# Performance work log

Measured on AMD Instinct MI355X. Metric: run time of the kernel, lower is better.

The kernel has to match this reference:

```python
import jax, jax.numpy as jnp
import numpy as np

DX = 0.1  # grid spacing (init arg dx); dy == dx
NX = 4096
NY = 4096


def _pad_bc(X, left, right, top, bottom):
    # X: [1, 1, Nx, Ny]; pad last axis with left/right values, then second-to-last with top/bottom.
    B, C, Nx, Ny = X.shape
    l = jnp.broadcast_to(left, (B, C, Nx, 1)).astype(X.dtype)
    r = jnp.broadcast_to(right, (B, C, Nx, 1)).astype(X.dtype)
    X = jnp.concatenate([l, X, r], axis=3)
    t = jnp.broadcast_to(top, (B, C, 1, Ny + 2)).astype(X.dtype)
    bo = jnp.broadcast_to(bottom, (B, C, 1, Ny + 2)).astype(X.dtype)
    return jnp.concatenate([t, X, bo], axis=2)


def _laplacian(Xp):
    # 5-point stencil, equivalent to conv2d with [[0,1,0],[1,-4,1],[0,1,0]]/dx^2 (valid padding).
    inv_dx2 = 1.0 / (DX * DX)
    return (
        Xp[:, :, :-2, 1:-1]
        + Xp[:, :, 2:, 1:-1]
        + Xp[:, :, 1:-1, :-2]
        + Xp[:, :, 1:-1, 2:]
        - 4.0 * Xp[:, :, 1:-1, 1:-1]
    ) * inv_dx2


def setup_inputs() -> dict:
    key = jax.random.key(0)
    k1, k2 = jax.random.split(key)
    state = jax.random.normal(k1, (1, 2, NX, NY), dtype=jnp.float32)
    bc = jax.random.uniform(k2, (1, 2, 4), dtype=jnp.float32)
    a_org = jnp.asarray(-2.0, dtype=jnp.float32)
    b_org = jnp.asarray(-2.0, dtype=jnp.float32)
    k_org = jnp.asarray(-2.0, dtype=jnp.float32)
    return {"state": state, "bc": bc, "a_org": a_org, "b_org": b_org, "k_org": k_org}


def reference(state, bc, a_org, b_org, k_org):
    a = jax.nn.sigmoid(a_org) * 0.01
    b = jax.nn.sigmoid(b_org) * 0.01
    k = jax.nn.sigmoid(k_org) * 0.01

    U = state[:, :1]  # [1,1,Nx,Ny]
    V = state[:, 1:]

    U_ = _pad_bc(U, bc[0, 0, 0], bc[0, 0, 1], bc[0, 0, 2], bc[0, 0, 3])
    V_ = _pad_bc(V, bc[0, 1, 0], bc[0, 1, 1], bc[0, 1, 2], bc[0, 1, 3])

    delta_u = _laplacian(U_)
    delta_v = _laplacian(V_)

    dUdt = a * delta_u + U - U ** 3 - V - k
    dVdt = b * delta_v + U - V
    return jnp.concatenate([dUdt, dVdt], axis=1)
```

## Files before the change

kernel.cpp:

```cpp
#include <hip/hip_runtime.h>

#define NXD 4096
#define NYD 4096

typedef float f32x4 __attribute__((ext_vector_type(4)));

__global__ __launch_bounds__(256) void DiffReactParamPDE_85478439125433_kernel(
    const float* __restrict__ state,
    const float* __restrict__ bc,
    const float* __restrict__ a_org,
    const float* __restrict__ b_org,
    const float* __restrict__ k_org,
    float* __restrict__ out)
{
    const float inv_dx2 = 100.0f;

    const int lane = threadIdx.x & 63;
    const int j0 = (blockIdx.x * 256 + threadIdx.x) * 4;
    const int i0 = blockIdx.y * 2;

    const float* __restrict__ U = state;
    const float* __restrict__ V = state + (size_t)NXD * NYD;
    float* __restrict__ dU = out;
    float* __restrict__ dV = out + (size_t)NXD * NYD;

    const int rT = (i0 == 0) ? 0 : i0 - 1;
    const int rB = (i0 + 2 >= NXD) ? NXD - 1 : i0 + 2;

#define LD4(P, ROW) (*(const float4*)((P) + (size_t)(ROW) * NYD + j0))
    float4 um = LD4(U, rT);
    float4 u0 = LD4(U, i0);
    float4 u1 = LD4(U, i0 + 1);
    float4 up = LD4(U, rB);
    float4 vm = LD4(V, rT);
    float4 v0 = LD4(V, i0);
    float4 v1 = LD4(V, i0 + 1);
    float4 vp = LD4(V, rB);
#undef LD4

    const float uL = bc[0], uR = bc[1], uT = bc[2], uB = bc[3];
    const float vL = bc[4], vR = bc[5], vT = bc[6], vB = bc[7];

    float eLu0 = uL, eLu1 = uL, eLv0 = vL, eLv1 = vL;
    float eRu0 = uR, eRu1 = uR, eRv0 = vR, eRv1 = vR;
    if (lane == 0 && j0 > 0) {
        eLu0 = U[(size_t)i0 * NYD + j0 - 1];
        eLu1 = U[(size_t)(i0 + 1) * NYD + j0 - 1];
        eLv0 = V[(size_t)i0 * NYD + j0 - 1];
        eLv1 = V[(size_t)(i0 + 1) * NYD + j0 - 1];
    }
    if (lane == 63 && j0 + 4 < NYD) {
        eRu0 = U[(size_t)i0 * NYD + j0 + 4];
        eRu1 = U[(size_t)(i0 + 1) * NYD + j0 + 4];
        eRv0 = V[(size_t)i0 * NYD + j0 + 4];
        eRv1 = V[(size_t)(i0 + 1) * NYD + j0 + 4];
    }

    const float a = 0.01f / (1.0f + expf(-a_org[0]));
    const float b = 0.01f / (1.0f + expf(-b_org[0]));
    const float k = 0.01f / (1.0f + expf(-k_org[0]));

    if (i0 == 0) {
        um = make_float4(uT, uT, uT, uT);
        vm = make_float4(vT, vT, vT, vT);
    }
    if (i0 + 2 >= NXD) {
        up = make_float4(uB, uB, uB, uB);
        vp = make_float4(vB, vB, vB, vB);
    }

    {
        float ulft = __shfl_up(u0.w, 1);   if (lane == 0)  ulft = eLu0;
        float urgt = __shfl_down(u0.x, 1); if (lane == 63) urgt = eRu0;
        float vlft = __shfl_up(v0.w, 1);   if (lane == 0)  vlft = eLv0;
        float vrgt = __shfl_down(v0.x, 1); if (lane == 63) vrgt = eRv0;

        const float lu0 = (um.x + u1.x + ulft + u0.y - 4.0f * u0.x) * inv_dx2;
        const float lu1 = (um.y + u1.y + u0.x + u0.z - 4.0f * u0.y) * inv_dx2;
        const float lu2 = (um.z + u1.z + u0.y + u0.w - 4.0f * u0.z) * inv_dx2;
        const float lu3 = (um.w + u1.w + u0.z + urgt - 4.0f * u0.w) * inv_dx2;

        const float lv0 = (vm.x + v1.x + vlft + v0.y - 4.0f * v0.x) * inv_dx2;
        const float lv1 = (vm.y + v1.y + v0.x + v0.z - 4.0f * v0.y) * inv_dx2;
        const float lv2 = (vm.z + v1.z + v0.y + v0.w - 4.0f * v0.z) * inv_dx2;
        const float lv3 = (vm.w + v1.w + v0.z + vrgt - 4.0f * v0.w) * inv_dx2;

        f32x4 duo, dvo;
        duo.x = a * lu0 + u0.x - u0.x * u0.x * u0.x - v0.x - k;
        duo.y = a * lu1 + u0.y - u0.y * u0.y * u0.y - v0.y - k;
        duo.z = a * lu2 + u0.z - u0.z * u0.z * u0.z - v0.z - k;
        duo.w = a * lu3 + u0.w - u0.w * u0.w * u0.w - v0.w - k;

        dvo.x = b * lv0 + u0.x - v0.x;
        dvo.y = b * lv1 + u0.y - v0.y;
        dvo.z = b * lv2 + u0.z - v0.z;
        dvo.w = b * lv3 + u0.w - v0.w;

        const size_t bo = (size_t)i0 * NYD + j0;
        __builtin_nontemporal_store(duo, (f32x4*)(dU + bo));
        __builtin_nontemporal_store(dvo, (f32x4*)(dV + bo));
    }

    {
        float ulft = __shfl_up(u1.w, 1);   if (lane == 0)  ulft = eLu1;
        float urgt = __shfl_down(u1.x, 1); if (lane == 63) urgt = eRu1;
        float vlft = __shfl_up(v1.w, 1);   if (lane == 0)  vlft = eLv1;
        float vrgt = __shfl_down(v1.x, 1); if (lane == 63) vrgt = eRv1;

        const float lu0 = (u0.x + up.x + ulft + u1.y - 4.0f * u1.x) * inv_dx2;
        const float lu1 = (u0.y + up.y + u1.x + u1.z - 4.0f * u1.y) * inv_dx2;
        const float lu2 = (u0.z + up.z + u1.y + u1.w - 4.0f * u1.z) * inv_dx2;
        const float lu3 = (u0.w + up.w + u1.z + urgt - 4.0f * u1.w) * inv_dx2;

        const float lv0 = (v0.x + vp.x + vlft + v1.y - 4.0f * v1.x) * inv_dx2;
        const float lv1 = (v0.y + vp.y + v1.x + v1.z - 4.0f * v1.y) * inv_dx2;
        const float lv2 = (v0.z + vp.z + v1.y + v1.w - 4.0f * v1.z) * inv_dx2;
        const float lv3 = (v0.w + vp.w + v1.z + vrgt - 4.0f * v1.w) * inv_dx2;

        f32x4 duo, dvo;
        duo.x = a * lu0 + u1.x - u1.x * u1.x * u1.x - v1.x - k;
        duo.y = a * lu1 + u1.y - u1.y * u1.y * u1.y - v1.y - k;
        duo.z = a * lu2 + u1.z - u1.z * u1.z * u1.z - v1.z - k;
        duo.w = a * lu3 + u1.w - u1.w * u1.w * u1.w - v1.w - k;

        dvo.x = b * lv0 + u1.x - v1.x;
        dvo.y = b * lv1 + u1.y - v1.y;
        dvo.z = b * lv2 + u1.z - v1.z;
        dvo.w = b * lv3 + u1.w - v1.w;

        const size_t bo = (size_t)(i0 + 1) * NYD + j0;
        __builtin_nontemporal_store(duo, (f32x4*)(dU + bo));
        __builtin_nontemporal_store(dvo, (f32x4*)(dV + bo));
    }
}

extern "C" void kernel_launch(void* const* d_in, const int* in_sizes, int n_in,
                              void* d_out, int out_size, void* d_ws, size_t ws_size,
                              hipStream_t stream) {
    const float* state = (const float*)d_in[0];
    const float* bc    = (const float*)d_in[1];
    const float* a_org = (const float*)d_in[2];
    const float* b_org = (const float*)d_in[3];
    const float* k_org = (const float*)d_in[4];
    float* out = (float*)d_out;

    dim3 block(256, 1, 1);
    dim3 grid(NYD / (4 * 256), NXD / 2, 1);
    DiffReactParamPDE_85478439125433_kernel<<<grid, block, 0, stream>>>(
        state, bc, a_org, b_org, k_org, out);
}
```

Measured before the change: 236.5 us.

## Cover full rows per block and exchange horizontal halos via shared memory

Each block of 1024 threads now spans an entire 4096-wide row pair, so left/right neighbours come from shared memory instead of wavefront shuffles plus scattered scalar global loads at wave edges. This removes the extra uncoalesced edge loads and the per-wave boundary special-casing. In exchange it adds a 32 KB shared buffer, a block-wide barrier, and larger blocks that may lower occupancy on a bandwidth-bound kernel.

```diff
diff --git a/kernel.cpp b/kernel.cpp
--- a/kernel.cpp
+++ b/kernel.cpp
@@ -5,7 +5,7 @@
 
 typedef float f32x4 __attribute__((ext_vector_type(4)));
 
-__global__ __launch_bounds__(256) void DiffReactParamPDE_85478439125433_kernel(
+__global__ __launch_bounds__(1024) void DiffReactParamPDE_85478439125433_kernel(
     const float* __restrict__ state,
     const float* __restrict__ bc,
     const float* __restrict__ a_org,
@@ -15,9 +15,9 @@
 {
     const float inv_dx2 = 100.0f;
 
-    const int lane = threadIdx.x & 63;
-    const int j0 = (blockIdx.x * 256 + threadIdx.x) * 4;
-    const int i0 = blockIdx.y * 2;
+    const int tid = threadIdx.x;
+    const int j0  = tid * 4;
+    const int i0  = blockIdx.x * 2;
 
     const float* __restrict__ U = state;
     const float* __restrict__ V = state + (size_t)NXD * NYD;
@@ -41,24 +41,27 @@
     const float uL = bc[0], uR = bc[1], uT = bc[2], uB = bc[3];
     const float vL = bc[4], vR = bc[5], vT = bc[6], vB = bc[7];
 
-    float eLu0 = uL, eLu1 = uL, eLv0 = vL, eLv1 = vL;
-    float eRu0 = uR, eRu1 = uR, eRv0 = vR, eRv1 = vR;
-    if (lane == 0 && j0 > 0) {
-        eLu0 = U[(size_t)i0 * NYD + j0 - 1];
-        eLu1 = U[(size_t)(i0 + 1) * NYD + j0 - 1];
-        eLv0 = V[(size_t)i0 * NYD + j0 - 1];
-        eLv1 = V[(size_t)(i0 + 1) * NYD + j0 - 1];
-    }
-    if (lane == 63 && j0 + 4 < NYD) {
-        eRu0 = U[(size_t)i0 * NYD + j0 + 4];
-        eRu1 = U[(size_t)(i0 + 1) * NYD + j0 + 4];
-        eRv0 = V[(size_t)i0 * NYD + j0 + 4];
-        eRv1 = V[(size_t)(i0 + 1) * NYD + j0 + 4];
-    }
-
     const float a = 0.01f / (1.0f + expf(-a_org[0]));
     const float b = 0.01f / (1.0f + expf(-b_org[0]));
     const float k = 0.01f / (1.0f + expf(-k_org[0]));
+
+    __shared__ float sx[8][1024];
+    sx[0][tid] = u0.x;  sx[1][tid] = u0.w;
+    sx[2][tid] = u1.x;  sx[3][tid] = u1.w;
+    sx[4][tid] = v0.x;  sx[5][tid] = v0.w;
+    sx[6][tid] = v1.x;  sx[7][tid] = v1.w;
+    __syncthreads();
+
+    const int tm = (tid == 0)    ? 0    : tid - 1;
+    const int tp = (tid == 1023) ? 1023 : tid + 1;
+    float ulft0 = (tid == 0)    ? uL : sx[1][tm];
+    float urgt0 = (tid == 1023) ? uR : sx[0][tp];
+    float ulft1 = (tid == 0)    ? uL : sx[3][tm];
+    float urgt1 = (tid == 1023) ? uR : sx[2][tp];
+    float vlft0 = (tid == 0)    ? vL : sx[5][tm];
+    float vrgt0 = (tid == 1023) ? vR : sx[4][tp];
+    float vlft1 = (tid == 0)    ? vL : sx[7][tm];
+    float vrgt1 = (tid == 1023) ? vR : sx[6][tp];
 
     if (i0 == 0) {
         um = make_float4(uT, uT, uT, uT);
@@ -70,20 +73,15 @@
     }
 
     {
-        float ulft = __shfl_up(u0.w, 1);   if (lane == 0)  ulft = eLu0;
-        float urgt = __shfl_down(u0.x, 1); if (lane == 63) urgt = eRu0;
-        float vlft = __shfl_up(v0.w, 1);   if (lane == 0)  vlft = eLv0;
-        float vrgt = __shfl_down(v0.x, 1); if (lane == 63) vrgt = eRv0;
+        const float lu0 = (um.x + u1.x + ulft0 + u0.y - 4.0f * u0.x) * inv_dx2;
+        const float lu1 = (um.y + u1.y + u0.x  + u0.z - 4.0f * u0.y) * inv_dx2;
+        const float lu2 = (um.z + u1.z + u0.y  + u0.w - 4.0f * u0.z) * inv_dx2;
+        const float lu3 = (um.w + u1.w + u0.z  + urgt0 - 4.0f * u0.w) * inv_dx2;
 
-        const float lu0 = (um.x + u1.x + ulft + u0.y - 4.0f * u0.x) * inv_dx2;
-        const float lu1 = (um.y + u1.y + u0.x + u0.z - 4.0f * u0.y) * inv_dx2;
-        const float lu2 = (um.z + u1.z + u0.y + u0.w - 4.0f * u0.z) * inv_dx2;
-        const float lu3 = (um.w + u1.w + u0.z + urgt - 4.0f * u0.w) * inv_dx2;
-
-        const float lv0 = (vm.x + v1.x + vlft + v0.y - 4.0f * v0.x) * inv_dx2;
-        const float lv1 = (vm.y + v1.y + v0.x + v0.z - 4.0f * v0.y) * inv_dx2;
-        const float lv2 = (vm.z + v1.z + v0.y + v0.w - 4.0f * v0.z) * inv_dx2;
-        const float lv3 = (vm.w + v1.w + v0.z + vrgt - 4.0f * v0.w) * inv_dx2;
+        const float lv0 = (vm.x + v1.x + vlft0 + v0.y - 4.0f * v0.x) * inv_dx2;
+        const float lv1 = (vm.y + v1.y + v0.x  + v0.z - 4.0f * v0.y) * inv_dx2;
+        const float lv2 = (vm.z + v1.z + v0.y  + v0.w - 4.0f * v0.z) * inv_dx2;
+        const float lv3 = (vm.w + v1.w + v0.z  + vrgt0 - 4.0f * v0.w) * inv_dx2;
 
         f32x4 duo, dvo;
         duo.x = a * lu0 + u0.x - u0.x * u0.x * u0.x - v0.x - k;
@@ -102,20 +100,15 @@
     }
 
     {
-        float ulft = __shfl_up(u1.w, 1);   if (lane == 0)  ulft = eLu1;
-        float urgt = __shfl_down(u1.x, 1); if (lane == 63) urgt = eRu1;
-        float vlft = __shfl_up(v1.w, 1);   if (lane == 0)  vlft = eLv1;
-        float vrgt = __shfl_down(v1.x, 1); if (lane == 63) vrgt = eRv1;
+        const float lu0 = (u0.x + up.x + ulft1 + u1.y - 4.0f * u1.x) * inv_dx2;
+        const float lu1 = (u0.y + up.y + u1.x  + u1.z - 4.0f * u1.y) * inv_dx2;
+        const float lu2 = (u0.z + up.z + u1.y  + u1.w - 4.0f * u1.z) * inv_dx2;
+        const float lu3 = (u0.w + up.w + u1.z  + urgt1 - 4.0f * u1.w) * inv_dx2;
 
-        const float lu0 = (u0.x + up.x + ulft + u1.y - 4.0f * u1.x) * inv_dx2;
-        const float lu1 = (u0.y + up.y + u1.x + u1.z - 4.0f * u1.y) * inv_dx2;
-        const float lu2 = (u0.z + up.z + u1.y + u1.w - 4.0f * u1.z) * inv_dx2;
-        const float lu3 = (u0.w + up.w + u1.z + urgt - 4.0f * u1.w) * inv_dx2;
-
-        const float lv0 = (v0.x + vp.x + vlft + v1.y - 4.0f * v1.x) * inv_dx2;
-        const float lv1 = (v0.y + vp.y + v1.x + v1.z - 4.0f * v1.y) * inv_dx2;
-        const float lv2 = (v0.z + vp.z + v1.y + v1.w - 4.0f * v1.z) * inv_dx2;
-        const float lv3 = (v0.w + vp.w + v1.z + vrgt - 4.0f * v1.w) * inv_dx2;
+        const float lv0 = (v0.x + vp.x + vlft1 + v1.y - 4.0f * v1.x) * inv_dx2;
+        const float lv1 = (v0.y + vp.y + v1.x  + v1.z - 4.0f * v1.y) * inv_dx2;
+        const float lv2 = (v0.z + vp.z + v1.y  + v1.w - 4.0f * v1.z) * inv_dx2;
+        const float lv3 = (v0.w + vp.w + v1.z  + vrgt1 - 4.0f * v1.w) * inv_dx2;
 
         f32x4 duo, dvo;
         duo.x = a * lu0 + u1.x - u1.x * u1.x * u1.x - v1.x - k;
@@ -144,8 +137,8 @@
     const float* k_org = (const float*)d_in[4];
     float* out = (float*)d_out;
 
-    dim3 block(256, 1, 1);
-    dim3 grid(NYD / (4 * 256), NXD / 2, 1);
+    dim3 block(1024, 1, 1);
+    dim3 grid(NXD / 2, 1, 1);
     DiffReactParamPDE_85478439125433_kernel<<<grid, block, 0, stream>>>(
         state, bc, a_org, b_org, k_org, out);
 }
```

Measured after the change: 242.7 us. 2.6% more time.
